# Kernel optimization log

Hardware: AMD Instinct MI355X
Metric: run time of the kernel (lower is better)

## Reference

```python
import jax, jax.numpy as jnp
import numpy as np

ALPHA = 0.1        # self.alpha in the torch module
NUM_CLASSES = 10   # predict_acc hardcodes range(10)


def _sqdist(x, centers):
    # Faithful to sum((x - c)**2, -1) but computed via the gemm identity to
    # avoid materializing the (N, K, D) broadcast the torch code creates.
    x2 = jnp.sum(x * x, axis=1, keepdims=True)          # [N, 1]
    c2 = jnp.sum(centers * centers, axis=1)             # [K]
    d = x2 + c2[None, :] - 2.0 * (x @ centers.T)        # [N, K]
    return jnp.maximum(d, 0.0)                          # clamp fp round-off


def _predict_acc(distance, y):
    n = distance.shape[0]
    y_p = jnp.argmin(distance, axis=1)                  # index[1][:, 0]
    # counts[i, c] = #points assigned to cluster i (only i < 10 matter) with label c
    onehot_cluster = (y_p[:, None] == jnp.arange(NUM_CLASSES)[None, :]).astype(jnp.float32)  # [N, 10]
    onehot_label = (y[:, None] == jnp.arange(NUM_CLASSES)[None, :]).astype(jnp.float32)      # [N, 10]
    counts = onehot_cluster.T @ onehot_label            # [10, 10]
    used = jnp.zeros((NUM_CLASSES,), dtype=bool)
    correct = jnp.float32(0.0)
    for i in range(NUM_CLASSES):
        bin_i = counts[i]
        has_points = jnp.sum(bin_i) > 0                 # empty bincount -> 'continue'
        label = jnp.argmax(bin_i)                       # first max index, like where(bin==max)[0][0]
        # quchong: recursively zero already-used labels == argmax with used masked out
        masked = jnp.where(used, 0.0, bin_i)
        label = jnp.where(used[label], jnp.argmax(masked), label)
        correct = correct + jnp.where(has_points, bin_i[label], 0.0)
        used = jnp.where(has_points, used.at[label].set(True), used)
    return correct / jnp.float32(n)


def setup_inputs() -> dict:
    key = jax.random.key(0)
    kx, ky, kc = jax.random.split(key, 3)
    N, K, D = 262144, 256, 64
    x = jax.random.normal(kx, (N, D), dtype=jnp.float32)
    y = jax.random.randint(ky, (N,), 0, 10, dtype=jnp.int64)
    centers = jax.random.normal(kc, (K, D), dtype=jnp.float32)
    return {"x": x, "y": y, "centers": centers}


def reference(x, y, centers):
    distance = _sqdist(x, centers)                      # caldis, op='l2'
    # calwei: exp(-alpha*log(d+1)) then row-normalize
    we = jnp.exp(-ALPHA * jnp.log1p(distance))
    weight = we / jnp.sum(we, axis=1, keepdims=True)
    loss = jnp.sum(weight * distance)                   # calloss
    acc = _predict_acc(distance, y)
    return (loss, acc)
```

## Files before the change

### kernel.cpp

```cpp
#include <hip/hip_runtime.h>

#define ALPHA 0.1f
#define NUM_CLASSES 10

typedef __attribute__((ext_vector_type(8))) short bf16x8;
typedef __attribute__((ext_vector_type(4))) float f32x4;


__device__ __forceinline__ unsigned pack2(float a, float b) {
    return (__float_as_uint(b) & 0xFFFF0000u) | (__float_as_uint(a) >> 16);
}
__device__ __forceinline__ float truncbf(float a) {
    return __uint_as_float(__float_as_uint(a) & 0xFFFF0000u);
}


__global__ __launch_bounds__(512, 4) void dist_kernel(
    const float* __restrict__ x,
    const int*   __restrict__ y,
    const float* __restrict__ centers,
    float* __restrict__ loss_acc,
    unsigned int* __restrict__ counts,
    int NT)
{
    __shared__ __align__(16) char bstage[4 * 4 * 64 * 16];
    __shared__ float x2s[64];
    __shared__ float c2s[256];
    __shared__ float    comb_swe[8][64];
    __shared__ float    comb_swd[8][64];
    __shared__ unsigned comb_best[8][64];

    const int tid  = threadIdx.x;
    const int w    = tid >> 6;
    const int lane = tid & 63;
    const int q    = lane >> 4;
    const int r    = lane & 15;

    if (tid < 256) {
        const float4* crow = (const float4*)(centers + tid * 64);
        float s = 0.f;
#pragma unroll
        for (int j = 0; j < 16; ++j) {
            float4 v = crow[j];
            s = fmaf(v.x, v.x, s); s = fmaf(v.y, v.y, s);
            s = fmaf(v.z, v.z, s); s = fmaf(v.w, v.w, s);
        }
        c2s[tid] = s;
    }

    bf16x8 af[2][4];
#pragma unroll
    for (int ct = 0; ct < 2; ++ct) {
        const int row = w * 32 + ct * 16 + r;
        const float4* C = (const float4*)(centers + (size_t)row * 64);
        float4 v0 = C[q * 2], v1 = C[q * 2 + 1];
        float4 v2 = C[8 + q * 2], v3 = C[9 + q * 2];
        union { bf16x8 v; unsigned u[4]; } h0, h1, l0, l1;
        h0.u[0] = pack2(v0.x, v0.y); h0.u[1] = pack2(v0.z, v0.w);
        h0.u[2] = pack2(v1.x, v1.y); h0.u[3] = pack2(v1.z, v1.w);
        h1.u[0] = pack2(v2.x, v2.y); h1.u[1] = pack2(v2.z, v2.w);
        h1.u[2] = pack2(v3.x, v3.y); h1.u[3] = pack2(v3.z, v3.w);
        l0.u[0] = pack2(v0.x - truncbf(v0.x), v0.y - truncbf(v0.y));
        l0.u[1] = pack2(v0.z - truncbf(v0.z), v0.w - truncbf(v0.w));
        l0.u[2] = pack2(v1.x - truncbf(v1.x), v1.y - truncbf(v1.y));
        l0.u[3] = pack2(v1.z - truncbf(v1.z), v1.w - truncbf(v1.w));
        l1.u[0] = pack2(v2.x - truncbf(v2.x), v2.y - truncbf(v2.y));
        l1.u[1] = pack2(v2.z - truncbf(v2.z), v2.w - truncbf(v2.w));
        l1.u[2] = pack2(v3.x - truncbf(v3.x), v3.y - truncbf(v3.y));
        l1.u[3] = pack2(v3.z - truncbf(v3.z), v3.w - truncbf(v3.w));
        af[ct][0] = h0.v; af[ct][1] = h1.v; af[ct][2] = l0.v; af[ct][3] = l1.v;
    }
    __syncthreads();

    float c2r[2][4];
#pragma unroll
    for (int ct = 0; ct < 2; ++ct) {
        float4 v = *(const float4*)(c2s + w * 32 + ct * 16 + q * 4);
        c2r[ct][0] = v.x; c2r[ct][1] = v.y; c2r[ct][2] = v.z; c2r[ct][3] = v.w;
    }

    float loss_local = 0.f;

    for (int t = blockIdx.x; t < NT; t += gridDim.x) {
        if (w < 4) {
            const int row = t * 64 + w * 16 + r;
            const float4* X = (const float4*)(x + (size_t)row * 64);
            float4 v0 = X[q * 2], v1 = X[q * 2 + 1];
            float4 v2 = X[8 + q * 2], v3 = X[9 + q * 2];

            float p = v0.x * v0.x;
            p = fmaf(v0.y, v0.y, p); p = fmaf(v0.z, v0.z, p); p = fmaf(v0.w, v0.w, p);
            p = fmaf(v1.x, v1.x, p); p = fmaf(v1.y, v1.y, p); p = fmaf(v1.z, v1.z, p); p = fmaf(v1.w, v1.w, p);
            p = fmaf(v2.x, v2.x, p); p = fmaf(v2.y, v2.y, p); p = fmaf(v2.z, v2.z, p); p = fmaf(v2.w, v2.w, p);
            p = fmaf(v3.x, v3.x, p); p = fmaf(v3.y, v3.y, p); p = fmaf(v3.z, v3.z, p); p = fmaf(v3.w, v3.w, p);
            p += __shfl_xor(p, 16);
            p += __shfl_xor(p, 32);
            if (q == 0) x2s[w * 16 + r] = p;

            union { bf16x8 v; uint4 u4; unsigned u[4]; } h0, h1, l0, l1;
            h0.u[0] = pack2(v0.x, v0.y); h0.u[1] = pack2(v0.z, v0.w);
            h0.u[2] = pack2(v1.x, v1.y); h0.u[3] = pack2(v1.z, v1.w);
            h1.u[0] = pack2(v2.x, v2.y); h1.u[1] = pack2(v2.z, v2.w);
            h1.u[2] = pack2(v3.x, v3.y); h1.u[3] = pack2(v3.z, v3.w);
            l0.u[0] = pack2(v0.x - truncbf(v0.x), v0.y - truncbf(v0.y));
            l0.u[1] = pack2(v0.z - truncbf(v0.z), v0.w - truncbf(v0.w));
            l0.u[2] = pack2(v1.x - truncbf(v1.x), v1.y - truncbf(v1.y));
            l0.u[3] = pack2(v1.z - truncbf(v1.z), v1.w - truncbf(v1.w));
            l1.u[0] = pack2(v2.x - truncbf(v2.x), v2.y - truncbf(v2.y));
            l1.u[1] = pack2(v2.z - truncbf(v2.z), v2.w - truncbf(v2.w));
            l1.u[2] = pack2(v3.x - truncbf(v3.x), v3.y - truncbf(v3.y));
            l1.u[3] = pack2(v3.z - truncbf(v3.z), v3.w - truncbf(v3.w));
            *(uint4*)(bstage + (((w * 4 + 0) * 64 + lane) << 4)) = h0.u4;
            *(uint4*)(bstage + (((w * 4 + 1) * 64 + lane) << 4)) = h1.u4;
            *(uint4*)(bstage + (((w * 4 + 2) * 64 + lane) << 4)) = l0.u4;
            *(uint4*)(bstage + (((w * 4 + 3) * 64 + lane) << 4)) = l1.u4;
        }
        __syncthreads();

#pragma unroll
        for (int pt = 0; pt < 4; ++pt) {
            union { uint4 u4; bf16x8 v; } b0, b1, b2, b3;
            b0.u4 = *(const uint4*)(bstage + (((pt * 4 + 0) * 64 + lane) << 4));
            b1.u4 = *(const uint4*)(bstage + (((pt * 4 + 1) * 64 + lane) << 4));
            b2.u4 = *(const uint4*)(bstage + (((pt * 4 + 2) * 64 + lane) << 4));
            b3.u4 = *(const uint4*)(bstage + (((pt * 4 + 3) * 64 + lane) << 4));
            const float x2p = x2s[pt * 16 + r];

            f32x4 acc[2];
#pragma unroll
            for (int ct = 0; ct < 2; ++ct) {
                f32x4 a = (f32x4){0.f, 0.f, 0.f, 0.f};
                a = __builtin_amdgcn_mfma_f32_16x16x32_bf16(af[ct][0], b0.v, a, 0, 0, 0);
                a = __builtin_amdgcn_mfma_f32_16x16x32_bf16(af[ct][1], b1.v, a, 0, 0, 0);
                a = __builtin_amdgcn_mfma_f32_16x16x32_bf16(af[ct][2], b0.v, a, 0, 0, 0);
                a = __builtin_amdgcn_mfma_f32_16x16x32_bf16(af[ct][3], b1.v, a, 0, 0, 0);
                a = __builtin_amdgcn_mfma_f32_16x16x32_bf16(af[ct][0], b2.v, a, 0, 0, 0);
                a = __builtin_amdgcn_mfma_f32_16x16x32_bf16(af[ct][1], b3.v, a, 0, 0, 0);
                acc[ct] = a;
            }

            float swe = 0.f, swd = 0.f;
            unsigned best = 0xFFFFFFFFu;
#pragma unroll
            for (int ct = 0; ct < 2; ++ct) {
#pragma unroll
                for (int reg = 0; reg < 4; ++reg) {
                    float d = fmaf(-2.f, acc[ct][reg], x2p + c2r[ct][reg]);
                    d = fmaxf(d, 0.f);
                    const unsigned kid = (unsigned)(w * 32 + ct * 16 + q * 4 + reg);
                    unsigned u = (__float_as_uint(d) & 0xFFFFFF00u) | kid;
                    best = min(best, u);
                    float wg = exp2f(-ALPHA * __log2f(1.f + d));
                    swe += wg;
                    swd = fmaf(wg, d, swd);
                }
            }
            swe += __shfl_xor(swe, 16); swe += __shfl_xor(swe, 32);
            swd += __shfl_xor(swd, 16); swd += __shfl_xor(swd, 32);
            best = min(best, (unsigned)__shfl_xor((int)best, 16));
            best = min(best, (unsigned)__shfl_xor((int)best, 32));
            if (q == 0) {
                comb_swe[w][pt * 16 + r] = swe;
                comb_swd[w][pt * 16 + r] = swd;
                comb_best[w][pt * 16 + r] = best;
            }
        }
        __syncthreads();

        if (tid < 64) {
            float SWE = comb_swe[0][tid], SWD = comb_swd[0][tid];
            unsigned BEST = comb_best[0][tid];
#pragma unroll
            for (int g = 1; g < 8; ++g) {
                SWE += comb_swe[g][tid];
                SWD += comb_swd[g][tid];
                BEST = min(BEST, comb_best[g][tid]);
            }
            loss_local += SWD / SWE;
            const unsigned bk = BEST & 0xFFu;
            if (bk < NUM_CLASSES) {
                const int lbl = y[t * 64 + tid];
                atomicAdd(&counts[bk * NUM_CLASSES + lbl], 1u);
            }
        }
    }

    if (w == 0) {
        float v = loss_local;
#pragma unroll
        for (int o = 32; o > 0; o >>= 1) v += __shfl_down(v, o);
        if (lane == 0) atomicAdd(loss_acc, v);
    }
}


__global__ void finalize_kernel(
    const float* __restrict__ loss_acc,
    const unsigned int* __restrict__ counts,
    float* __restrict__ out,
    int N)
{
    if (threadIdx.x == 0 && blockIdx.x == 0) {
        float c[NUM_CLASSES][NUM_CLASSES];
        for (int i = 0; i < NUM_CLASSES; ++i)
            for (int j = 0; j < NUM_CLASSES; ++j)
                c[i][j] = (float)counts[i * NUM_CLASSES + j];

        bool used[NUM_CLASSES];
        for (int i = 0; i < NUM_CLASSES; ++i) used[i] = false;

        float correct = 0.f;
        for (int i = 0; i < NUM_CLASSES; ++i) {
            float rowsum = 0.f;
            for (int j = 0; j < NUM_CLASSES; ++j) rowsum += c[i][j];
            bool has_points = rowsum > 0.f;

            int label = 0;
            float mx = c[i][0];
            for (int j = 1; j < NUM_CLASSES; ++j)
                if (c[i][j] > mx) { mx = c[i][j]; label = j; }

            if (used[label]) {
                float mm = used[0] ? 0.f : c[i][0];
                int l2 = 0;
                for (int j = 1; j < NUM_CLASSES; ++j) {
                    float v = used[j] ? 0.f : c[i][j];
                    if (v > mm) { mm = v; l2 = j; }
                }
                label = l2;
            }

            if (has_points) {
                correct += c[i][label];
                used[label] = true;
            }
        }
        out[0] = loss_acc[0];
        out[1] = correct / (float)N;
    }
}


extern "C" void kernel_launch(void* const* d_in, const int* in_sizes, int n_in,
                              void* d_out, int out_size, void* d_ws, size_t ws_size,
                              hipStream_t stream)
{
    const float* x       = (const float*)d_in[0];
    const int*   y       = (const int*)d_in[1];
    const float* centers = (const float*)d_in[2];
    float* out = (float*)d_out;

    const int N  = in_sizes[0] / 64;
    const int NT = N / 64;

    float* loss          = (float*)d_ws;
    unsigned int* counts = (unsigned int*)((char*)d_ws + 4);

    hipMemsetAsync(d_ws, 0, 512, stream);

    int grid = 512;
    if (grid > NT) grid = NT;
    dist_kernel<<<grid, 512, 0, stream>>>(x, y, centers, loss, counts, NT);

    finalize_kernel<<<1, 64, 0, stream>>>(loss, counts, out, N);
}
```

Baseline: 153.3 us.

## Fuse finalize into main kernel, split staging across waves, parallelize combine

Folds the finalize step into the distance kernel: the last block to finish, detected with an atomic counter, computes the accuracy and writes the outputs, which removes one kernel launch. Staging work is split so waves 0-3 produce the bf16 high parts and x² while waves 4-7 produce the low residual parts. The per-row cross-wave combine now runs on all 512 threads with shuffles instead of 64 threads looping, and every wave contributes to the loss atomics. The grid is doubled to 1024 blocks, which adds more atomic contention and a serial tail in the last block.

```diff
diff --git a/kernel.cpp b/kernel.cpp
--- a/kernel.cpp
+++ b/kernel.cpp
@@ -21,7 +21,9 @@
     const float* __restrict__ centers,
     float* __restrict__ loss_acc,
     unsigned int* __restrict__ counts,
-    int NT)
+    unsigned int* __restrict__ done,
+    float* __restrict__ out,
+    int N, int NT)
 {
     __shared__ __align__(16) char bstage[4 * 4 * 64 * 16];
     __shared__ float x2s[64];
@@ -37,7 +39,7 @@
     const int r    = lane & 15;
 
     if (tid < 256) {
-        const float4* crow = (const float4*)(centers + tid * 64);
+        const float4* crow = (const float4*)(centers + (size_t)tid * 64);
         float s = 0.f;
 #pragma unroll
         for (int j = 0; j < 16; ++j) {
@@ -82,38 +84,43 @@
     float loss_local = 0.f;
 
     for (int t = blockIdx.x; t < NT; t += gridDim.x) {
-        if (w < 4) {
-            const int row = t * 64 + w * 16 + r;
+        {
+            const int sw = w & 3;
+            const int row = t * 64 + sw * 16 + r;
             const float4* X = (const float4*)(x + (size_t)row * 64);
             float4 v0 = X[q * 2], v1 = X[q * 2 + 1];
             float4 v2 = X[8 + q * 2], v3 = X[9 + q * 2];
 
-            float p = v0.x * v0.x;
-            p = fmaf(v0.y, v0.y, p); p = fmaf(v0.z, v0.z, p); p = fmaf(v0.w, v0.w, p);
-            p = fmaf(v1.x, v1.x, p); p = fmaf(v1.y, v1.y, p); p = fmaf(v1.z, v1.z, p); p = fmaf(v1.w, v1.w, p);
-            p = fmaf(v2.x, v2.x, p); p = fmaf(v2.y, v2.y, p); p = fmaf(v2.z, v2.z, p); p = fmaf(v2.w, v2.w, p);
-            p = fmaf(v3.x, v3.x, p); p = fmaf(v3.y, v3.y, p); p = fmaf(v3.z, v3.z, p); p = fmaf(v3.w, v3.w, p);
-            p += __shfl_xor(p, 16);
-            p += __shfl_xor(p, 32);
-            if (q == 0) x2s[w * 16 + r] = p;
-
-            union { bf16x8 v; uint4 u4; unsigned u[4]; } h0, h1, l0, l1;
-            h0.u[0] = pack2(v0.x, v0.y); h0.u[1] = pack2(v0.z, v0.w);
-            h0.u[2] = pack2(v1.x, v1.y); h0.u[3] = pack2(v1.z, v1.w);
-            h1.u[0] = pack2(v2.x, v2.y); h1.u[1] = pack2(v2.z, v2.w);
-            h1.u[2] = pack2(v3.x, v3.y); h1.u[3] = pack2(v3.z, v3.w);
-            l0.u[0] = pack2(v0.x - truncbf(v0.x), v0.y - truncbf(v0.y));
-            l0.u[1] = pack2(v0.z - truncbf(v0.z), v0.w - truncbf(v0.w));
-            l0.u[2] = pack2(v1.x - truncbf(v1.x), v1.y - truncbf(v1.y));
-            l0.u[3] = pack2(v1.z - truncbf(v1.z), v1.w - truncbf(v1.w));
-            l1.u[0] = pack2(v2.x - truncbf(v2.x), v2.y - truncbf(v2.y));
-            l1.u[1] = pack2(v2.z - truncbf(v2.z), v2.w - truncbf(v2.w));
-            l1.u[2] = pack2(v3.x - truncbf(v3.x), v3.y - truncbf(v3.y));
-            l1.u[3] = pack2(v3.z - truncbf(v3.z), v3.w - truncbf(v3.w));
-            *(uint4*)(bstage + (((w * 4 + 0) * 64 + lane) << 4)) = h0.u4;
-            *(uint4*)(bstage + (((w * 4 + 1) * 64 + lane) << 4)) = h1.u4;
-            *(uint4*)(bstage + (((w * 4 + 2) * 64 + lane) << 4)) = l0.u4;
-            *(uint4*)(bstage + (((w * 4 + 3) * 64 + lane) << 4)) = l1.u4;
+            if (w < 4) {
+                float p = v0.x * v0.x;
+                p = fmaf(v0.y, v0.y, p); p = fmaf(v0.z, v0.z, p); p = fmaf(v0.w, v0.w, p);
+                p = fmaf(v1.x, v1.x, p); p = fmaf(v1.y, v1.y, p); p = fmaf(v1.z, v1.z, p); p = fmaf(v1.w, v1.w, p);
+                p = fmaf(v2.x, v2.x, p); p = fmaf(v2.y, v2.y, p); p = fmaf(v2.z, v2.z, p); p = fmaf(v2.w, v2.w, p);
+                p = fmaf(v3.x, v3.x, p); p = fmaf(v3.y, v3.y, p); p = fmaf(v3.z, v3.z, p); p = fmaf(v3.w, v3.w, p);
+                p += __shfl_xor(p, 16);
+                p += __shfl_xor(p, 32);
+                if (q == 0) x2s[sw * 16 + r] = p;
+
+                union { bf16x8 v; uint4 u4; unsigned u[4]; } h0, h1;
+                h0.u[0] = pack2(v0.x, v0.y); h0.u[1] = pack2(v0.z, v0.w);
+                h0.u[2] = pack2(v1.x, v1.y); h0.u[3] = pack2(v1.z, v1.w);
+                h1.u[0] = pack2(v2.x, v2.y); h1.u[1] = pack2(v2.z, v2.w);
+                h1.u[2] = pack2(v3.x, v3.y); h1.u[3] = pack2(v3.z, v3.w);
+                *(uint4*)(bstage + (((sw * 4 + 0) * 64 + lane) << 4)) = h0.u4;
+                *(uint4*)(bstage + (((sw * 4 + 1) * 64 + lane) << 4)) = h1.u4;
+            } else {
+                union { bf16x8 v; uint4 u4; unsigned u[4]; } l0, l1;
+                l0.u[0] = pack2(v0.x - truncbf(v0.x), v0.y - truncbf(v0.y));
+                l0.u[1] = pack2(v0.z - truncbf(v0.z), v0.w - truncbf(v0.w));
+                l0.u[2] = pack2(v1.x - truncbf(v1.x), v1.y - truncbf(v1.y));
+                l0.u[3] = pack2(v1.z - truncbf(v1.z), v1.w - truncbf(v1.w));
+                l1.u[0] = pack2(v2.x - truncbf(v2.x), v2.y - truncbf(v2.y));
+                l1.u[1] = pack2(v2.z - truncbf(v2.z), v2.w - truncbf(v2.w));
+                l1.u[2] = pack2(v3.x - truncbf(v3.x), v3.y - truncbf(v3.y));
+                l1.u[3] = pack2(v3.z - truncbf(v3.z), v3.w - truncbf(v3.w));
+                *(uint4*)(bstage + (((sw * 4 + 2) * 64 + lane) << 4)) = l0.u4;
+                *(uint4*)(bstage + (((sw * 4 + 3) * 64 + lane) << 4)) = l1.u4;
+            }
         }
         __syncthreads();
 
@@ -167,76 +174,76 @@
         }
         __syncthreads();
 
-        if (tid < 64) {
-            float SWE = comb_swe[0][tid], SWD = comb_swd[0][tid];
-            unsigned BEST = comb_best[0][tid];
-#pragma unroll
-            for (int g = 1; g < 8; ++g) {
-                SWE += comb_swe[g][tid];
-                SWD += comb_swd[g][tid];
-                BEST = min(BEST, comb_best[g][tid]);
-            }
-            loss_local += SWD / SWE;
-            const unsigned bk = BEST & 0xFFu;
-            if (bk < NUM_CLASSES) {
-                const int lbl = y[t * 64 + tid];
-                atomicAdd(&counts[bk * NUM_CLASSES + lbl], 1u);
-            }
-        }
-    }
-
-    if (w == 0) {
+        {
+            const int p = tid >> 3;
+            const int g = tid & 7;
+            float SWE = comb_swe[g][p];
+            float SWD = comb_swd[g][p];
+            unsigned B = comb_best[g][p];
+            SWE += __shfl_xor(SWE, 1); SWE += __shfl_xor(SWE, 2); SWE += __shfl_xor(SWE, 4);
+            SWD += __shfl_xor(SWD, 1); SWD += __shfl_xor(SWD, 2); SWD += __shfl_xor(SWD, 4);
+            B = min(B, (unsigned)__shfl_xor((int)B, 1));
+            B = min(B, (unsigned)__shfl_xor((int)B, 2));
+            B = min(B, (unsigned)__shfl_xor((int)B, 4));
+            if (g == 0) {
+                loss_local += SWD / SWE;
+                const unsigned bk = B & 0xFFu;
+                if (bk < NUM_CLASSES) {
+                    const int lbl = y[t * 64 + p];
+                    atomicAdd(&counts[bk * NUM_CLASSES + lbl], 1u);
+                }
+            }
+        }
+    }
+
+    {
         float v = loss_local;
 #pragma unroll
         for (int o = 32; o > 0; o >>= 1) v += __shfl_down(v, o);
         if (lane == 0) atomicAdd(loss_acc, v);
     }
-}
-
-
-__global__ void finalize_kernel(
-    const float* __restrict__ loss_acc,
-    const unsigned int* __restrict__ counts,
-    float* __restrict__ out,
-    int N)
-{
-    if (threadIdx.x == 0 && blockIdx.x == 0) {
-        float c[NUM_CLASSES][NUM_CLASSES];
-        for (int i = 0; i < NUM_CLASSES; ++i)
-            for (int j = 0; j < NUM_CLASSES; ++j)
-                c[i][j] = (float)counts[i * NUM_CLASSES + j];
-
-        bool used[NUM_CLASSES];
-        for (int i = 0; i < NUM_CLASSES; ++i) used[i] = false;
-
-        float correct = 0.f;
-        for (int i = 0; i < NUM_CLASSES; ++i) {
-            float rowsum = 0.f;
-            for (int j = 0; j < NUM_CLASSES; ++j) rowsum += c[i][j];
-            bool has_points = rowsum > 0.f;
-
-            int label = 0;
-            float mx = c[i][0];
-            for (int j = 1; j < NUM_CLASSES; ++j)
-                if (c[i][j] > mx) { mx = c[i][j]; label = j; }
-
-            if (used[label]) {
-                float mm = used[0] ? 0.f : c[i][0];
-                int l2 = 0;
-                for (int j = 1; j < NUM_CLASSES; ++j) {
-                    float v = used[j] ? 0.f : c[i][j];
-                    if (v > mm) { mm = v; l2 = j; }
-                }
-                label = l2;
-            }
-
-            if (has_points) {
-                correct += c[i][label];
-                used[label] = true;
-            }
-        }
-        out[0] = loss_acc[0];
-        out[1] = correct / (float)N;
+
+    __syncthreads();
+    if (tid == 0) {
+        __threadfence();
+        if (atomicAdd(done, 1u) == gridDim.x - 1) {
+            __threadfence();
+            float c[NUM_CLASSES][NUM_CLASSES];
+            for (int i = 0; i < NUM_CLASSES; ++i)
+                for (int j = 0; j < NUM_CLASSES; ++j)
+                    c[i][j] = (float)atomicAdd(&counts[i * NUM_CLASSES + j], 0u);
+            const float L = atomicAdd(loss_acc, 0.f);
+
+            bool used[NUM_CLASSES];
+            for (int i = 0; i < NUM_CLASSES; ++i) used[i] = false;
+            float correct = 0.f;
+            for (int i = 0; i < NUM_CLASSES; ++i) {
+                float rowsum = 0.f;
+                for (int j = 0; j < NUM_CLASSES; ++j) rowsum += c[i][j];
+                const bool has_points = rowsum > 0.f;
+
+                int label = 0;
+                float mx = c[i][0];
+                for (int j = 1; j < NUM_CLASSES; ++j)
+                    if (c[i][j] > mx) { mx = c[i][j]; label = j; }
+
+                if (used[label]) {
+                    float mm = used[0] ? 0.f : c[i][0];
+                    int l2 = 0;
+                    for (int j = 1; j < NUM_CLASSES; ++j) {
+                        float vv = used[j] ? 0.f : c[i][j];
+                        if (vv > mm) { mm = vv; l2 = j; }
+                    }
+                    label = l2;
+                }
+                if (has_points) {
+                    correct += c[i][label];
+                    used[label] = true;
+                }
+            }
+            out[0] = L;
+            out[1] = correct / (float)N;
+        }
     }
 }
 
@@ -255,12 +262,12 @@
 
     float* loss          = (float*)d_ws;
     unsigned int* counts = (unsigned int*)((char*)d_ws + 4);
+    unsigned int* done   = (unsigned int*)((char*)d_ws + 404);
 
     hipMemsetAsync(d_ws, 0, 512, stream);
 
-    int grid = 512;
+    int grid = 1024;
     if (grid > NT) grid = NT;
-    dist_kernel<<<grid, 512, 0, stream>>>(x, y, centers, loss, counts, NT);
-
-    finalize_kernel<<<1, 64, 0, stream>>>(loss, counts, out, N);
-}
+    dist_kernel<<<grid, 512, 0, stream>>>(x, y, centers, loss, counts,
+                                          done, out, N, NT);
+}
```

New measurement: 258.6 us. 1.69x slower.
